# Kernel tuning notes

Measured on AMD Instinct MI355X. Metric: run time of the kernel, lower is better.

## Reference

```python
import jax, jax.numpy as jnp
import numpy as np

N_NODES = 50000
N_EDGES = 1600000
IN_DIM, HID_DIM, OUT_DIM = 512, 128, 16


def spmm(edge_src, edge_dst, edge_vals, x):
    # sparse.mm(A, x): out[dst] += A[dst, src] * x[src]
    msgs = edge_vals[:, None] * x[edge_src]  # [E, D]
    return jax.ops.segment_sum(msgs, edge_dst, num_segments=N_NODES)


def setup_inputs() -> dict:
    key = jax.random.key(0)
    k1, k2, k3, k4, k5, k6 = jax.random.split(key, 6)
    feature = jax.random.normal(k1, (N_NODES, IN_DIM), dtype=jnp.float32)
    edge_src = jax.random.randint(k2, (N_EDGES,), 0, N_NODES, dtype=jnp.int32)
    edge_dst = jax.random.randint(k3, (N_EDGES,), 0, N_NODES, dtype=jnp.int32)
    edge_vals = jax.random.uniform(k4, (N_EDGES,), dtype=jnp.float32)
    # kaiming_uniform-style init: bound = sqrt(6 / fan_in) (a=sqrt(5) omitted for simplicity of scale)
    b1 = float(np.sqrt(6.0 / IN_DIM))
    b2 = float(np.sqrt(6.0 / HID_DIM))
    W1 = jax.random.uniform(k5, (IN_DIM, HID_DIM), dtype=jnp.float32, minval=-b1, maxval=b1)
    W2 = jax.random.uniform(k6, (HID_DIM, OUT_DIM), dtype=jnp.float32, minval=-b2, maxval=b2)
    return {"feature": feature, "edge_src": edge_src, "edge_dst": edge_dst,
            "edge_vals": edge_vals, "W1": W1, "W2": W2}


def reference(feature, edge_src, edge_dst, edge_vals, W1, W2):
    # layer 1: dense matmul -> sparse aggregation -> ReLU
    h = jax.nn.relu(spmm(edge_src, edge_dst, edge_vals, feature @ W1))
    # layer 2
    out = spmm(edge_src, edge_dst, edge_vals, h @ W2)
    return out
```

## Files before the change

### kernel.cpp

```cpp
#include <hip/hip_runtime.h>

#define N_NODES 50000
#define N_EDGES 1600000
#define IN_DIM 512
#define HID_DIM 128
#define OUT_DIM 16

#define BKT_SHIFT 6
#define BKT_NODES 64
#define NB ((N_NODES + BKT_NODES - 1) / BKT_NODES)
#define SC_BLOCKS ((N_EDGES + 4095) / 4096)
#define PREP_BLOCKS ((IN_DIM * HID_DIM + 1023) / 1024)
#define NS_CAP 2560

typedef __attribute__((ext_vector_type(8))) __bf16 bf16x8;
typedef __attribute__((ext_vector_type(4))) __bf16 bf16x4;
typedef __attribute__((ext_vector_type(8))) unsigned short ushort8;
typedef __attribute__((ext_vector_type(4))) float f32x4;
typedef __attribute__((ext_vector_type(2))) float f32x2;

static __device__ __forceinline__ unsigned short f2bf(float x) {
    unsigned int u = __float_as_uint(x);
    u += 0x7FFFu + ((u >> 16) & 1u);
    return (unsigned short)(u >> 16);
}
static __device__ __forceinline__ float bf2f(unsigned short v) {
    return __uint_as_float(((unsigned int)v) << 16);
}
static __device__ __forceinline__ unsigned char f2fp8(float x) {
    int pk = __builtin_amdgcn_cvt_pk_fp8_f32(x, x, 0, false);
    return (unsigned char)(pk & 0xFF);
}

__device__ inline int wave_incl_scan(int v) {
    #pragma unroll
    for (int off = 1; off < 64; off <<= 1) {
        int x = __shfl_up(v, off, 64);
        if ((threadIdx.x & 63) >= off) v += x;
    }
    return v;
}


__global__ void zero_bcnt_kernel(int* __restrict__ bcnt) {
    int t = threadIdx.x;
    if (t < NB) bcnt[t] = 0;
}

__global__ __launch_bounds__(1024) void hist_prep_kernel(const int* __restrict__ dst,
                                                         int* __restrict__ bcnt,
                                                         const float* __restrict__ W1,
                                                         unsigned short* __restrict__ Wt) {
    if (blockIdx.x >= SC_BLOCKS) {
        int i = (blockIdx.x - SC_BLOCKS) * 1024 + threadIdx.x;
        if (i < IN_DIM * HID_DIM) {
            int k = i >> 7, col = i & 127;
            Wt[(size_t)col * IN_DIM + k] = f2bf(W1[i]);
        }
        return;
    }
    __shared__ int lc[NB];
    const int t = threadIdx.x;
    for (int b = t; b < NB; b += 1024) lc[b] = 0;
    __syncthreads();
    const int e0 = blockIdx.x * 4096;
    #pragma unroll
    for (int i = 0; i < 4; i++) {
        int e = e0 + i * 1024 + t;
        if (e < N_EDGES) atomicAdd(&lc[dst[e] >> BKT_SHIFT], 1);
    }
    __syncthreads();
    for (int b = t; b < NB; b += 1024)
        if (lc[b]) atomicAdd(&bcnt[b], lc[b]);
}

__global__ __launch_bounds__(1024) void bucket_scan_kernel(const int* __restrict__ bcnt,
                                                           int* __restrict__ bucket_ptr,
                                                           int* __restrict__ cursor) {
    __shared__ int wsums[16];
    const int t = threadIdx.x;
    const int lane = t & 63, wid = t >> 6;
    int v = (t < NB) ? bcnt[t] : 0;
    int incl = wave_incl_scan(v);
    if (lane == 63) wsums[wid] = incl;
    __syncthreads();
    if (wid == 0) {
        int wv = (lane < 16) ? wsums[lane] : 0;
        int ws = wave_incl_scan(wv);
        if (lane < 16) wsums[lane] = ws;
    }
    __syncthreads();
    int woff = wid ? wsums[wid - 1] : 0;
    int excl = woff + incl - v;
    if (t < NB) { bucket_ptr[t] = excl; cursor[t] = excl; }
    if (t == NB - 1) bucket_ptr[NB] = excl + v;
}

__global__ __launch_bounds__(1024) void bucket_scatter_kernel(const int* __restrict__ src,
                                                              const int* __restrict__ dst,
                                                              const float* __restrict__ val,
                                                              int* __restrict__ cursor,
                                                              int2* __restrict__ pairs_bkt) {
    __shared__ int cnt[NB];
    __shared__ int bbase[NB];
    const int t = threadIdx.x;
    const int e0 = blockIdx.x * 4096;
    for (int b = t; b < NB; b += 1024) cnt[b] = 0;
    __syncthreads();
    #pragma unroll
    for (int i = 0; i < 4; i++) {
        int e = e0 + i * 1024 + t;
        if (e < N_EDGES) atomicAdd(&cnt[dst[e] >> BKT_SHIFT], 1);
    }
    __syncthreads();
    for (int b = t; b < NB; b += 1024) {
        int c = cnt[b];
        bbase[b] = c ? atomicAdd(&cursor[b], c) : 0;
        cnt[b] = 0;
    }
    __syncthreads();
    #pragma unroll
    for (int i = 0; i < 4; i++) {
        int e = e0 + i * 1024 + t;
        if (e < N_EDGES) {
            int dd = dst[e];
            int b = dd >> BKT_SHIFT, dl = dd & (BKT_NODES - 1);
            int pos = bbase[b] + atomicAdd(&cnt[b], 1);
            int2 pr;
            pr.x = src[e] | (dl << 16);
            pr.y = __float_as_int(val[e]);
            pairs_bkt[pos] = pr;
        }
    }
}

__global__ __launch_bounds__(512) void node_sort_fused_kernel(const int2* __restrict__ pairs_bkt,
                                                              const int* __restrict__ bucket_ptr,
                                                              int* __restrict__ row_ptr,
                                                              int2* __restrict__ pairs) {
    __shared__ int cnt[BKT_NODES];
    __shared__ int base[BKT_NODES];
    __shared__ int2 stage[NS_CAP];
    const int t = threadIdx.x;
    const int b = blockIdx.x;
    const int s = bucket_ptr[b], e = bucket_ptr[b + 1];
    if (t < BKT_NODES) cnt[t] = 0;
    __syncthreads();
    for (int i = s + t; i < e; i += 512)
        atomicAdd(&cnt[pairs_bkt[i].x >> 16], 1);
    __syncthreads();
    if (t < BKT_NODES) {
        int v = cnt[t];
        int incl = wave_incl_scan(v);
        base[t] = s + incl - v;
    }
    __syncthreads();
    if (t < BKT_NODES) {
        int n = b * BKT_NODES + t;
        if (n < N_NODES) row_ptr[n] = base[t];
        cnt[t] = 0;
    }
    if (b == NB - 1 && t == 0) row_ptr[N_NODES] = N_EDGES;
    __syncthreads();
    for (int i = s + t; i < e; i += 512) {
        int2 pr = pairs_bkt[i];
        int dl = pr.x >> 16;
        int p = base[dl] + atomicAdd(&cnt[dl], 1);
        int loc = p - s;
        if (loc < NS_CAP) stage[loc] = pr;
        else pairs[p] = pr;
    }
    __syncthreads();
    const int lim = min(e - s, NS_CAP);
    for (int j = t; j < lim; j += 512)
        pairs[s + j] = stage[j];
}


#define G1_XSTR 72
#define G1_BSTR 72
__global__ __launch_bounds__(256) void gemm1_kernel(const float* __restrict__ X,
                                                    const unsigned short* __restrict__ Wt,
                                                    unsigned char* __restrict__ h0) {
    __shared__ __align__(16) unsigned short Xs[64 * G1_XSTR];
    __shared__ __align__(16) unsigned short Bs[128 * G1_BSTR];
    const int t = threadIdx.x;
    const int lane = t & 63;
    const int wave = t >> 6;
    const int c = lane & 15, g = lane >> 4;
    const int m0 = blockIdx.x * 64;

    f32x4 acc[4][2];
    #pragma unroll
    for (int mt = 0; mt < 4; mt++)
        #pragma unroll
        for (int nt = 0; nt < 2; nt++) acc[mt][nt] = (f32x4){0.f, 0.f, 0.f, 0.f};

    float4 xr[4];
    ushort8 br[4];

    #define G1_LOAD(kt)                                                                  \
        _Pragma("unroll")                                                                \
        for (int p = 0; p < 4; p++) {                                                    \
            int idx = p * 256 + t;                                                       \
            int xrow = idx >> 4, xseg = idx & 15;                                        \
            int grow = m0 + xrow; grow = (grow < N_NODES) ? grow : (N_NODES - 1);        \
            xr[p] = *(const float4*)&X[(size_t)grow * IN_DIM + (kt) * 64 + xseg * 4];    \
            int bcol = idx >> 3, bseg = idx & 7;                                         \
            br[p] = *(const ushort8*)&Wt[(size_t)bcol * IN_DIM + (kt) * 64 + bseg * 8];  \
        }

    G1_LOAD(0)
    for (int kt = 0; kt < 8; kt++) {
        #pragma unroll
        for (int p = 0; p < 4; p++) {
            int idx = p * 256 + t;
            int xrow = idx >> 4, xseg = idx & 15;
            bf16x4 xw;
            xw[0] = (__bf16)xr[p].x; xw[1] = (__bf16)xr[p].y;
            xw[2] = (__bf16)xr[p].z; xw[3] = (__bf16)xr[p].w;
            *(bf16x4*)&Xs[xrow * G1_XSTR + xseg * 4] = xw;
            int bcol = idx >> 3, bseg = idx & 7;
            *(ushort8*)&Bs[bcol * G1_BSTR + bseg * 8] = br[p];
        }
        __syncthreads();
        if (kt < 7) G1_LOAD(kt + 1)
        #pragma unroll
        for (int ks = 0; ks < 2; ks++) {
            bf16x8 bf[2];
            #pragma unroll
            for (int nt = 0; nt < 2; nt++) {
                int col = wave * 32 + nt * 16 + c;
                bf[nt] = *(const bf16x8*)&Bs[col * G1_BSTR + ks * 32 + g * 8];
            }
            #pragma unroll
            for (int mt = 0; mt < 4; mt++) {
                bf16x8 af = *(const bf16x8*)&Xs[(mt * 16 + c) * G1_XSTR + ks * 32 + g * 8];
                #pragma unroll
                for (int nt = 0; nt < 2; nt++)
                    acc[mt][nt] = __builtin_amdgcn_mfma_f32_16x16x32_bf16(af, bf[nt],
                                                                          acc[mt][nt], 0, 0, 0);
            }
        }
        __syncthreads();
    }
    #undef G1_LOAD

    #pragma unroll
    for (int mt = 0; mt < 4; mt++) {
        #pragma unroll
        for (int r = 0; r < 4; r++) {
            int row = m0 + mt * 16 + g * 4 + r;
            if (row < N_NODES) {
                #pragma unroll
                for (int nt = 0; nt < 2; nt++) {
                    int col = wave * 32 + nt * 16 + c;
                    h0[(size_t)row * HID_DIM + col] = f2fp8(acc[mt][nt][r]);
                }
            }
        }
    }
}

__global__ __launch_bounds__(256) void spmm1_node_kernel(const unsigned char* __restrict__ h0,
                                                         const int* __restrict__ row_ptr,
                                                         const int2* __restrict__ pairs,
                                                         unsigned short* __restrict__ h) {
    const int wid = __builtin_amdgcn_readfirstlane(threadIdx.x >> 6);
    const int n = blockIdx.x * 4 + wid;
    const int lane = threadIdx.x & 63;
    const int s = row_ptr[n], e = row_ptr[n + 1];
    const unsigned char* h0l = h0 + lane * 2;
    float ax = 0.f, ay = 0.f;
    for (int base = s; base < e; base += 8) {
        float vv[8];
        const unsigned char* rp[8];
        #pragma unroll
        for (int k = 0; k < 8; k++) {
            int idx = base + k;
            int cidx = (idx < e) ? idx : (e - 1);
            int2 pr = pairs[cidx];
            vv[k] = (idx < e) ? __int_as_float(pr.y) : 0.f;
            rp[k] = h0l + (size_t)(pr.x & 0xFFFF) * HID_DIM;
        }
        unsigned short gg[8];
        #pragma unroll
        for (int k = 0; k < 8; k++) gg[k] = *(const unsigned short*)rp[k];
        #pragma unroll
        for (int k = 0; k < 8; k++) {
            f32x2 f = __builtin_amdgcn_cvt_pk_f32_fp8((int)gg[k], false);
            ax += vv[k] * f.x;
            ay += vv[k] * f.y;
        }
    }
    unsigned int w = ((unsigned int)f2bf(fmaxf(ay, 0.f)) << 16) | f2bf(fmaxf(ax, 0.f));
    ((unsigned int*)(h + (size_t)n * HID_DIM))[lane] = w;
}

__global__ __launch_bounds__(256) void gemm2_kernel(const unsigned short* __restrict__ H,
                                                    const float* __restrict__ W2,
                                                    unsigned short* __restrict__ C) {
    __shared__ float Hs[16][132];
    __shared__ float Ws[128][16];
    const int t = threadIdx.x;
    const int n0 = blockIdx.x * 16;
    #pragma unroll
    for (int p = 0; p < 2; p++) {
        int idx = p * 256 + t;
        ((float4*)Ws)[idx] = ((const float4*)W2)[idx];
    }
    {
        int row = t >> 4, seg = t & 15;
        int gr = n0 + row;
        ushort8 hv = {0, 0, 0, 0, 0, 0, 0, 0};
        if (gr < N_NODES) hv = *(const ushort8*)&H[(size_t)gr * HID_DIM + seg * 8];
        #pragma unroll
        for (int j = 0; j < 8; j++) Hs[row][seg * 8 + j] = bf2f(hv[j]);
    }
    __syncthreads();
    const int nl = t >> 4, j = t & 15;
    float acc = 0.f;
    #pragma unroll 8
    for (int k = 0; k < 128; k++) acc += Hs[nl][k] * Ws[k][j];
    int n = n0 + nl;
    if (n < N_NODES) C[(size_t)n * OUT_DIM + j] = f2bf(acc);
}

__global__ __launch_bounds__(256) void spmm2_node_kernel(const unsigned short* __restrict__ h2,
                                                         const int* __restrict__ row_ptr,
                                                         const int2* __restrict__ pairs,
                                                         float* __restrict__ out) {
    const int idx = blockIdx.x * 256 + threadIdx.x;
    const int n = idx >> 4;
    const int d = idx & 15;
    if (n >= N_NODES) return;
    const int s = row_ptr[n], e = row_ptr[n + 1];
    float acc = 0.f;
    int i = s;
    for (; i + 4 <= e; i += 4) {
        int2 p0 = pairs[i], p1 = pairs[i + 1], p2 = pairs[i + 2], p3 = pairs[i + 3];
        unsigned short g0 = h2[(size_t)(p0.x & 0xFFFF) * OUT_DIM + d];
        unsigned short g1 = h2[(size_t)(p1.x & 0xFFFF) * OUT_DIM + d];
        unsigned short g2 = h2[(size_t)(p2.x & 0xFFFF) * OUT_DIM + d];
        unsigned short g3 = h2[(size_t)(p3.x & 0xFFFF) * OUT_DIM + d];
        acc += __int_as_float(p0.y) * bf2f(g0) + __int_as_float(p1.y) * bf2f(g1)
             + __int_as_float(p2.y) * bf2f(g2) + __int_as_float(p3.y) * bf2f(g3);
    }
    for (; i < e; i++) {
        int2 pr = pairs[i];
        acc += __int_as_float(pr.y) * bf2f(h2[(size_t)(pr.x & 0xFFFF) * OUT_DIM + d]);
    }
    out[(size_t)n * OUT_DIM + d] = acc;
}


extern "C" void kernel_launch(void* const* d_in, const int* in_sizes, int n_in,
                              void* d_out, int out_size, void* d_ws, size_t ws_size,
                              hipStream_t stream) {
    const float* feature   = (const float*)d_in[0];
    const int*   edge_src  = (const int*)d_in[1];
    const int*   edge_dst  = (const int*)d_in[2];
    const float* edge_vals = (const float*)d_in[3];
    const float* W1        = (const float*)d_in[4];
    const float* W2        = (const float*)d_in[5];
    float* out = (float*)d_out;

    char* ws = (char*)d_ws;
    size_t off = 0;
    auto alloc = [&](size_t bytes) {
        void* p = ws + off;
        off += (bytes + 255) & ~(size_t)255;
        return p;
    };
    unsigned char*  h0    = (unsigned char*)alloc((size_t)N_NODES * HID_DIM);
    unsigned short* Wt    = (unsigned short*)alloc((size_t)IN_DIM * HID_DIM * 2);
    unsigned short* h     = (unsigned short*)alloc((size_t)N_NODES * HID_DIM * 2);
    unsigned short* h2    = (unsigned short*)alloc((size_t)N_NODES * OUT_DIM * 2);
    int*   bcnt           = (int*)alloc((size_t)NB * 4);
    int*   bucket_ptr     = (int*)alloc((size_t)(NB + 1) * 4);
    int*   cursor         = (int*)alloc((size_t)NB * 4);
    int*   row_ptr        = (int*)alloc((size_t)(N_NODES + 1) * 4);
    int2*  pairs_bkt      = (int2*)alloc((size_t)N_EDGES * 8);
    int2*  pairs          = (int2*)alloc((size_t)N_EDGES * 8);

    zero_bcnt_kernel<<<1, 1024, 0, stream>>>(bcnt);
    hist_prep_kernel<<<SC_BLOCKS + PREP_BLOCKS, 1024, 0, stream>>>(edge_dst, bcnt, W1, Wt);
    bucket_scan_kernel<<<1, 1024, 0, stream>>>(bcnt, bucket_ptr, cursor);
    bucket_scatter_kernel<<<SC_BLOCKS, 1024, 0, stream>>>(edge_src, edge_dst, edge_vals,
                                                          cursor, pairs_bkt);
    node_sort_fused_kernel<<<NB, 512, 0, stream>>>(pairs_bkt, bucket_ptr, row_ptr, pairs);

    gemm1_kernel<<<(N_NODES + 63) / 64, 256, 0, stream>>>(feature, Wt, h0);
    spmm1_node_kernel<<<(N_NODES + 3) / 4, 256, 0, stream>>>(h0, row_ptr, pairs, h);
    gemm2_kernel<<<(N_NODES + 15) / 16, 256, 0, stream>>>(h, W2, h2);
    spmm2_node_kernel<<<(N_NODES * 16 + 255) / 256, 256, 0, stream>>>(h2, row_ptr, pairs, out);
}
```

Measured before the change: 153.2 us.

## Precompute per-block bucket offsets and widen gemm1 tile to 128 rows

The histogram kernel now stores a per-block, per-bucket count matrix, and a new scan kernel turns it into exclusive offsets. The scatter kernel can then place edges without recounting them and without global cursor atomics. Edge loads are vectorized to int4/float4. Separately, gemm1 uses 512-thread blocks covering 128 rows, so each W tile load is shared by twice as many rows. The cost is an extra kernel launch and a roughly 1.25M-int histogram matrix write and read.

```diff
diff --git a/kernel.cpp b/kernel.cpp
--- a/kernel.cpp
+++ b/kernel.cpp
@@ -49,6 +49,7 @@
 
 __global__ __launch_bounds__(1024) void hist_prep_kernel(const int* __restrict__ dst,
                                                          int* __restrict__ bcnt,
+                                                         int* __restrict__ blk_hist_T,
                                                          const float* __restrict__ W1,
                                                          unsigned short* __restrict__ Wt) {
     if (blockIdx.x >= SC_BLOCKS) {
@@ -63,20 +64,29 @@
     const int t = threadIdx.x;
     for (int b = t; b < NB; b += 1024) lc[b] = 0;
     __syncthreads();
-    const int e0 = blockIdx.x * 4096;
-    #pragma unroll
-    for (int i = 0; i < 4; i++) {
-        int e = e0 + i * 1024 + t;
-        if (e < N_EDGES) atomicAdd(&lc[dst[e] >> BKT_SHIFT], 1);
-    }
-    __syncthreads();
-    for (int b = t; b < NB; b += 1024)
-        if (lc[b]) atomicAdd(&bcnt[b], lc[b]);
+    const int eb = blockIdx.x * 4096 + t * 4;
+    if (eb + 4 <= N_EDGES) {
+        int4 d4 = *(const int4*)&dst[eb];
+        atomicAdd(&lc[d4.x >> BKT_SHIFT], 1);
+        atomicAdd(&lc[d4.y >> BKT_SHIFT], 1);
+        atomicAdd(&lc[d4.z >> BKT_SHIFT], 1);
+        atomicAdd(&lc[d4.w >> BKT_SHIFT], 1);
+    } else {
+        for (int k = 0; k < 4; k++) {
+            int e = eb + k;
+            if (e < N_EDGES) atomicAdd(&lc[dst[e] >> BKT_SHIFT], 1);
+        }
+    }
+    __syncthreads();
+    for (int b = t; b < NB; b += 1024) {
+        int c = lc[b];
+        blk_hist_T[(size_t)b * SC_BLOCKS + blockIdx.x] = c;
+        if (c) atomicAdd(&bcnt[b], c);
+    }
 }
 
 __global__ __launch_bounds__(1024) void bucket_scan_kernel(const int* __restrict__ bcnt,
-                                                           int* __restrict__ bucket_ptr,
-                                                           int* __restrict__ cursor) {
+                                                           int* __restrict__ bucket_ptr) {
     __shared__ int wsums[16];
     const int t = threadIdx.x;
     const int lane = t & 63, wid = t >> 6;
@@ -92,44 +102,65 @@
     __syncthreads();
     int woff = wid ? wsums[wid - 1] : 0;
     int excl = woff + incl - v;
-    if (t < NB) { bucket_ptr[t] = excl; cursor[t] = excl; }
+    if (t < NB) bucket_ptr[t] = excl;
     if (t == NB - 1) bucket_ptr[NB] = excl + v;
+}
+
+__global__ __launch_bounds__(512) void base_scan_kernel(const int* __restrict__ bucket_ptr,
+                                                        int* __restrict__ blk_hist_T) {
+    const int lane = threadIdx.x & 63;
+    const int b = blockIdx.x * 8 + (threadIdx.x >> 6);
+    if (b >= NB) return;
+    int* row = blk_hist_T + (size_t)b * SC_BLOCKS;
+    int carry = bucket_ptr[b];
+    for (int c0 = 0; c0 < SC_BLOCKS; c0 += 64) {
+        int idx = c0 + lane;
+        int v = (idx < SC_BLOCKS) ? row[idx] : 0;
+        int incl = wave_incl_scan(v);
+        if (idx < SC_BLOCKS) row[idx] = carry + incl - v;
+        carry += __shfl(incl, 63, 64);
+    }
 }
 
 __global__ __launch_bounds__(1024) void bucket_scatter_kernel(const int* __restrict__ src,
                                                               const int* __restrict__ dst,
                                                               const float* __restrict__ val,
-                                                              int* __restrict__ cursor,
+                                                              const int* __restrict__ blk_hist_T,
                                                               int2* __restrict__ pairs_bkt) {
-    __shared__ int cnt[NB];
-    __shared__ int bbase[NB];
-    const int t = threadIdx.x;
-    const int e0 = blockIdx.x * 4096;
-    for (int b = t; b < NB; b += 1024) cnt[b] = 0;
-    __syncthreads();
-    #pragma unroll
-    for (int i = 0; i < 4; i++) {
-        int e = e0 + i * 1024 + t;
-        if (e < N_EDGES) atomicAdd(&cnt[dst[e] >> BKT_SHIFT], 1);
-    }
-    __syncthreads();
-    for (int b = t; b < NB; b += 1024) {
-        int c = cnt[b];
-        bbase[b] = c ? atomicAdd(&cursor[b], c) : 0;
-        cnt[b] = 0;
-    }
-    __syncthreads();
-    #pragma unroll
-    for (int i = 0; i < 4; i++) {
-        int e = e0 + i * 1024 + t;
-        if (e < N_EDGES) {
-            int dd = dst[e];
+    __shared__ int cbase[NB];
+    const int t = threadIdx.x;
+    for (int b = t; b < NB; b += 1024)
+        cbase[b] = blk_hist_T[(size_t)b * SC_BLOCKS + blockIdx.x];
+    __syncthreads();
+    const int eb = blockIdx.x * 4096 + t * 4;
+    if (eb + 4 <= N_EDGES) {
+        int4 s4 = *(const int4*)&src[eb];
+        int4 d4 = *(const int4*)&dst[eb];
+        float4 v4 = *(const float4*)&val[eb];
+        #pragma unroll
+        for (int k = 0; k < 4; k++) {
+            int ss = (k == 0) ? s4.x : (k == 1) ? s4.y : (k == 2) ? s4.z : s4.w;
+            int dd = (k == 0) ? d4.x : (k == 1) ? d4.y : (k == 2) ? d4.z : d4.w;
+            float vv = (k == 0) ? v4.x : (k == 1) ? v4.y : (k == 2) ? v4.z : v4.w;
             int b = dd >> BKT_SHIFT, dl = dd & (BKT_NODES - 1);
-            int pos = bbase[b] + atomicAdd(&cnt[b], 1);
+            int pos = atomicAdd(&cbase[b], 1);
             int2 pr;
-            pr.x = src[e] | (dl << 16);
-            pr.y = __float_as_int(val[e]);
+            pr.x = ss | (dl << 16);
+            pr.y = __float_as_int(vv);
             pairs_bkt[pos] = pr;
+        }
+    } else {
+        for (int k = 0; k < 4; k++) {
+            int e = eb + k;
+            if (e < N_EDGES) {
+                int dd = dst[e];
+                int b = dd >> BKT_SHIFT, dl = dd & (BKT_NODES - 1);
+                int pos = atomicAdd(&cbase[b], 1);
+                int2 pr;
+                pr.x = src[e] | (dl << 16);
+                pr.y = __float_as_int(val[e]);
+                pairs_bkt[pos] = pr;
+            }
         }
     }
 }
@@ -179,16 +210,18 @@
 
 #define G1_XSTR 72
 #define G1_BSTR 72
-__global__ __launch_bounds__(256) void gemm1_kernel(const float* __restrict__ X,
+__global__ __launch_bounds__(512) void gemm1_kernel(const float* __restrict__ X,
                                                     const unsigned short* __restrict__ Wt,
                                                     unsigned char* __restrict__ h0) {
-    __shared__ __align__(16) unsigned short Xs[64 * G1_XSTR];
+    __shared__ __align__(16) unsigned short Xs[128 * G1_XSTR];
     __shared__ __align__(16) unsigned short Bs[128 * G1_BSTR];
     const int t = threadIdx.x;
     const int lane = t & 63;
     const int wave = t >> 6;
+    const int wr = wave >> 2;
+    const int wc = wave & 3;
     const int c = lane & 15, g = lane >> 4;
-    const int m0 = blockIdx.x * 64;
+    const int m0 = blockIdx.x * 128;
 
     f32x4 acc[4][2];
     #pragma unroll
@@ -197,15 +230,19 @@
         for (int nt = 0; nt < 2; nt++) acc[mt][nt] = (f32x4){0.f, 0.f, 0.f, 0.f};
 
     float4 xr[4];
-    ushort8 br[4];
+    ushort8 br[2];
 
     #define G1_LOAD(kt)                                                                  \
         _Pragma("unroll")                                                                \
         for (int p = 0; p < 4; p++) {                                                    \
-            int idx = p * 256 + t;                                                       \
+            int idx = p * 512 + t;                                                       \
             int xrow = idx >> 4, xseg = idx & 15;                                        \
             int grow = m0 + xrow; grow = (grow < N_NODES) ? grow : (N_NODES - 1);        \
             xr[p] = *(const float4*)&X[(size_t)grow * IN_DIM + (kt) * 64 + xseg * 4];    \
+        }                                                                                \
+        _Pragma("unroll")                                                                \
+        for (int p = 0; p < 2; p++) {                                                    \
+            int idx = p * 512 + t;                                                       \
             int bcol = idx >> 3, bseg = idx & 7;                                         \
             br[p] = *(const ushort8*)&Wt[(size_t)bcol * IN_DIM + (kt) * 64 + bseg * 8];  \
         }
@@ -214,12 +251,16 @@
     for (int kt = 0; kt < 8; kt++) {
         #pragma unroll
         for (int p = 0; p < 4; p++) {
-            int idx = p * 256 + t;
+            int idx = p * 512 + t;
             int xrow = idx >> 4, xseg = idx & 15;
             bf16x4 xw;
             xw[0] = (__bf16)xr[p].x; xw[1] = (__bf16)xr[p].y;
             xw[2] = (__bf16)xr[p].z; xw[3] = (__bf16)xr[p].w;
             *(bf16x4*)&Xs[xrow * G1_XSTR + xseg * 4] = xw;
+        }
+        #pragma unroll
+        for (int p = 0; p < 2; p++) {
+            int idx = p * 512 + t;
             int bcol = idx >> 3, bseg = idx & 7;
             *(ushort8*)&Bs[bcol * G1_BSTR + bseg * 8] = br[p];
         }
@@ -230,12 +271,12 @@
             bf16x8 bf[2];
             #pragma unroll
             for (int nt = 0; nt < 2; nt++) {
-                int col = wave * 32 + nt * 16 + c;
+                int col = wc * 32 + nt * 16 + c;
                 bf[nt] = *(const bf16x8*)&Bs[col * G1_BSTR + ks * 32 + g * 8];
             }
             #pragma unroll
             for (int mt = 0; mt < 4; mt++) {
-                bf16x8 af = *(const bf16x8*)&Xs[(mt * 16 + c) * G1_XSTR + ks * 32 + g * 8];
+                bf16x8 af = *(const bf16x8*)&Xs[(wr * 64 + mt * 16 + c) * G1_XSTR + ks * 32 + g * 8];
                 #pragma unroll
                 for (int nt = 0; nt < 2; nt++)
                     acc[mt][nt] = __builtin_amdgcn_mfma_f32_16x16x32_bf16(af, bf[nt],
@@ -250,11 +291,11 @@
     for (int mt = 0; mt < 4; mt++) {
         #pragma unroll
         for (int r = 0; r < 4; r++) {
-            int row = m0 + mt * 16 + g * 4 + r;
+            int row = m0 + wr * 64 + mt * 16 + g * 4 + r;
             if (row < N_NODES) {
                 #pragma unroll
                 for (int nt = 0; nt < 2; nt++) {
-                    int col = wave * 32 + nt * 16 + c;
+                    int col = wc * 32 + nt * 16 + c;
                     h0[(size_t)row * HID_DIM + col] = f2fp8(acc[mt][nt][r]);
                 }
             }
@@ -378,19 +419,21 @@
     unsigned short* h2    = (unsigned short*)alloc((size_t)N_NODES * OUT_DIM * 2);
     int*   bcnt           = (int*)alloc((size_t)NB * 4);
     int*   bucket_ptr     = (int*)alloc((size_t)(NB + 1) * 4);
-    int*   cursor         = (int*)alloc((size_t)NB * 4);
+    int*   blk_hist_T     = (int*)alloc((size_t)NB * SC_BLOCKS * 4);
     int*   row_ptr        = (int*)alloc((size_t)(N_NODES + 1) * 4);
     int2*  pairs_bkt      = (int2*)alloc((size_t)N_EDGES * 8);
     int2*  pairs          = (int2*)alloc((size_t)N_EDGES * 8);
 
     zero_bcnt_kernel<<<1, 1024, 0, stream>>>(bcnt);
-    hist_prep_kernel<<<SC_BLOCKS + PREP_BLOCKS, 1024, 0, stream>>>(edge_dst, bcnt, W1, Wt);
-    bucket_scan_kernel<<<1, 1024, 0, stream>>>(bcnt, bucket_ptr, cursor);
+    hist_prep_kernel<<<SC_BLOCKS + PREP_BLOCKS, 1024, 0, stream>>>(edge_dst, bcnt, blk_hist_T,
+                                                                   W1, Wt);
+    bucket_scan_kernel<<<1, 1024, 0, stream>>>(bcnt, bucket_ptr);
+    base_scan_kernel<<<(NB + 7) / 8, 512, 0, stream>>>(bucket_ptr, blk_hist_T);
     bucket_scatter_kernel<<<SC_BLOCKS, 1024, 0, stream>>>(edge_src, edge_dst, edge_vals,
-                                                          cursor, pairs_bkt);
+                                                          blk_hist_T, pairs_bkt);
     node_sort_fused_kernel<<<NB, 512, 0, stream>>>(pairs_bkt, bucket_ptr, row_ptr, pairs);
 
-    gemm1_kernel<<<(N_NODES + 63) / 64, 256, 0, stream>>>(feature, Wt, h0);
+    gemm1_kernel<<<(N_NODES + 127) / 128, 512, 0, stream>>>(feature, Wt, h0);
     spmm1_node_kernel<<<(N_NODES + 3) / 4, 256, 0, stream>>>(h0, row_ptr, pairs, h);
     gemm2_kernel<<<(N_NODES + 15) / 16, 256, 0, stream>>>(h, W2, h2);
     spmm2_node_kernel<<<(N_NODES * 16 + 255) / 256, 256, 0, stream>>>(h2, row_ptr, pairs, out);
```

After: 146.5 us. -4.4%, faster.
